# Kernel tuning notes

Measured on AMD Instinct MI355X. Metric: run time of the kernel, lower is better.

The kernel has to match this reference:

```python
import jax, jax.numpy as jnp
import numpy as np

N_NODES = 1048576
N_GRAPHS = 4096
NODES_PER_GRAPH = N_NODES // N_GRAPHS
N_EDGES = 8388608
F_IN = 16
HID = 32


def _glorot(k, shp):
    return jax.random.normal(k, shp, jnp.float32) * np.float32(np.sqrt(2.0 / (shp[-2] + shp[-1])))


def setup_inputs() -> dict:
    key = jax.random.key(0)
    ks = jax.random.split(key, 8)
    d = F_IN + HID  # DCRNN gate convs act on cat([X, H])
    return {
        "x": jax.random.normal(ks[0], (N_NODES, F_IN), jnp.float32),
        "edge_index": jax.random.randint(ks[1], (2, N_EDGES), 0, N_NODES),
        "edge_weight": jax.random.uniform(ks[2], (N_EDGES,), jnp.float32),
        "batch": jnp.repeat(jnp.arange(N_GRAPHS), NODES_PER_GRAPH),
        "W_z": _glorot(ks[3], (2, 1, d, HID)),
        "b_z": jnp.zeros((HID,), jnp.float32),
        "W_r": _glorot(ks[4], (2, 1, d, HID)),
        "b_r": jnp.zeros((HID,), jnp.float32),
        "W_h": _glorot(ks[5], (2, 1, d, HID)),
        "b_h": jnp.zeros((HID,), jnp.float32),
        "W_lin": _glorot(ks[6], (HID, 1)),
        "b_lin": jnp.zeros((1,), jnp.float32),
    }


def _dconv_k1(X, W, b):
    # torch_geometric_temporal DConv with K=1: the diffusion loop never runs,
    # so H = X @ W[0,0] + X @ W[1,0] + b (edge_index/edge_weight unused).
    return X @ (W[0, 0] + W[1, 0]) + b


def reference(x, edge_index, edge_weight, batch, W_z, b_z, W_r, b_r, W_h, b_h, W_lin, b_lin):
    del edge_index, edge_weight  # mathematically unused when K=1
    h0 = jnp.zeros((x.shape[0], HID), x.dtype)  # DCRNN hidden state default
    xh = jnp.concatenate([x, h0], axis=1)
    Z = jax.nn.sigmoid(_dconv_k1(xh, W_z, b_z))
    R = jax.nn.sigmoid(_dconv_k1(xh, W_r, b_r))
    xhr = jnp.concatenate([x, h0 * R], axis=1)
    H_tilde = jnp.tanh(_dconv_k1(xhr, W_h, b_h))
    H = Z * h0 + (1.0 - Z) * H_tilde  # (N, 32)
    h = jax.nn.relu(H)
    h = h @ W_lin + b_lin  # (N, 1)
    # global_mean_pool over per-node graph ids
    sums = jax.ops.segment_sum(h, batch, num_segments=N_GRAPHS)
    cnts = jax.ops.segment_sum(jnp.ones((h.shape[0], 1), h.dtype), batch, num_segments=N_GRAPHS)
    return sums / jnp.maximum(cnts, 1.0)  # (N_GRAPHS, 1)
```

## Files before the change

### kernel.cpp

```cpp
#include <hip/hip_runtime.h>

#define N_NODES   1048576
#define N_GRAPHS  4096
#define NPG       256
#define F_IN      16
#define HID       32

#define WS_FLOATS 1121

__global__ __launch_bounds__(512) void prep_kernel(
    const float* __restrict__ Wz, const float* __restrict__ bz,
    const float* __restrict__ Wh, const float* __restrict__ bh,
    const float* __restrict__ Wlin, const float* __restrict__ blin,
    float* __restrict__ w)
{
    const int t = threadIdx.x;
    if (t < 512) {
        const int c = t >> 4;
        const int r = t & 15;
        const int src = r * HID + c;
        w[t]       = Wz[src] + Wz[1536 + src];
        w[512 + t] = Wh[src] + Wh[1536 + src];
    }
    if (t < HID) {
        w[1024 + t] = bz[t];
        w[1056 + t] = bh[t];
        w[1088 + t] = Wlin[t];
    }
    if (t == 0) w[1120] = blin[0];
}

__device__ __forceinline__ float node_forward(const float xv[F_IN], const float* __restrict__ w)
{
    float acc = 0.0f;
#pragma unroll 4
    for (int c = 0; c < HID; ++c) {
        float az = w[1024 + c];
        float ah = w[1056 + c];
#pragma unroll
        for (int r = 0; r < F_IN; ++r) {
            az = fmaf(xv[r], w[c * 16 + r],        az);
            ah = fmaf(xv[r], w[512 + c * 16 + r],  ah);
        }
        const float z  = 1.0f / (1.0f + __expf(-az));
        const float e  = __expf(2.0f * ah);
        const float th = 1.0f - 2.0f / (e + 1.0f);
        float H = (1.0f - z) * th;
        H = H > 0.0f ? H : 0.0f;
        acc = fmaf(H, w[1088 + c], acc);
    }
    return acc;
}

__device__ __forceinline__ void reduce_and_store(float acc, const float* w, float* out)
{
    const int t = threadIdx.x;
#pragma unroll
    for (int off = 32; off > 0; off >>= 1)
        acc += __shfl_down(acc, off, 64);
    __shared__ float part[4];
    if ((t & 63) == 0) part[t >> 6] = acc;
    __syncthreads();
    if (t == 0) {
        const float s = part[0] + part[1] + part[2] + part[3];
        out[blockIdx.x] = s * (1.0f / (float)NPG) + w[1120];
    }
}

__global__ __launch_bounds__(256) void gcn_main(
    const float* __restrict__ x, const float* __restrict__ w, float* __restrict__ out)
{
    const int node = blockIdx.x * NPG + threadIdx.x;
    const float4* xp = (const float4*)(x + (size_t)node * F_IN);
    const float4 a = xp[0], b = xp[1], c4 = xp[2], d4 = xp[3];
    const float xv[F_IN] = { a.x, a.y, a.z, a.w,  b.x, b.y, b.z, b.w,
                             c4.x, c4.y, c4.z, c4.w,  d4.x, d4.y, d4.z, d4.w };
    const float acc = node_forward(xv, w);
    reduce_and_store(acc, w, out);
}

__global__ __launch_bounds__(256) void gcn_main_lds(
    const float* __restrict__ x,
    const float* __restrict__ Wz, const float* __restrict__ bz,
    const float* __restrict__ Wh, const float* __restrict__ bh,
    const float* __restrict__ Wlin, const float* __restrict__ blin,
    float* __restrict__ out)
{
    __shared__ float w[WS_FLOATS];
    const int t = threadIdx.x;
#pragma unroll
    for (int i = t; i < 512; i += 256) {
        const int c = i >> 4, r = i & 15;
        const int src = r * HID + c;
        w[i]       = Wz[src] + Wz[1536 + src];
        w[512 + i] = Wh[src] + Wh[1536 + src];
    }
    if (t < HID) { w[1024 + t] = bz[t]; w[1056 + t] = bh[t]; w[1088 + t] = Wlin[t]; }
    if (t == 0)  w[1120] = blin[0];
    __syncthreads();

    const int node = blockIdx.x * NPG + t;
    const float4* xp = (const float4*)(x + (size_t)node * F_IN);
    const float4 a = xp[0], b = xp[1], c4 = xp[2], d4 = xp[3];
    const float xv[F_IN] = { a.x, a.y, a.z, a.w,  b.x, b.y, b.z, b.w,
                             c4.x, c4.y, c4.z, c4.w,  d4.x, d4.y, d4.z, d4.w };
    const float acc = node_forward(xv, w);
    reduce_and_store(acc, w, out);
}

extern "C" void kernel_launch(void* const* d_in, const int* in_sizes, int n_in,
                              void* d_out, int out_size, void* d_ws, size_t ws_size,
                              hipStream_t stream)
{
    const float* x    = (const float*)d_in[0];
    const float* Wz   = (const float*)d_in[4];
    const float* bz   = (const float*)d_in[5];
    const float* Wh   = (const float*)d_in[8];
    const float* bh   = (const float*)d_in[9];
    const float* Wlin = (const float*)d_in[10];
    const float* blin = (const float*)d_in[11];
    float* out = (float*)d_out;

    if (ws_size >= WS_FLOATS * sizeof(float)) {
        float* w = (float*)d_ws;
        prep_kernel<<<1, 512, 0, stream>>>(Wz, bz, Wh, bh, Wlin, blin, w);
        gcn_main<<<N_GRAPHS, NPG, 0, stream>>>(x, w, out);
    } else {
        gcn_main_lds<<<N_GRAPHS, NPG, 0, stream>>>(x, Wz, bz, Wh, bh, Wlin, blin, out);
    }
}
```

Baseline: 202.6 us.

## Process four nodes per thread to reuse weight loads across nodes

Each thread now handles four consecutive nodes, loading each weight column once into registers and applying it to all four nodes. This amortises the global/LDS weight reads per FMA and quarters the grid size. Each wavefront now covers exactly one graph, so the shared-memory cross-wave reduction and its barrier go away, and each wave stores its own graph mean. The per-thread x load becomes 16 float4 reads of strided rows, which is less coalesced, and the extra registers may lower occupancy.

```diff
diff --git a/kernel.cpp b/kernel.cpp
--- a/kernel.cpp
+++ b/kernel.cpp
@@ -5,6 +5,7 @@
 #define NPG       256
 #define F_IN      16
 #define HID       32
+#define NODES_PER_THREAD 4
 
 #define WS_FLOATS 1121
 
@@ -15,7 +16,7 @@
     float* __restrict__ w)
 {
     const int t = threadIdx.x;
-    if (t < 512) {
+    {
         const int c = t >> 4;
         const int r = t & 15;
         const int src = r * HID + c;
@@ -30,53 +31,65 @@
     if (t == 0) w[1120] = blin[0];
 }
 
-__device__ __forceinline__ float node_forward(const float xv[F_IN], const float* __restrict__ w)
+__device__ __forceinline__ void gcn_body(
+    const float* __restrict__ x, const float* w, float* __restrict__ out,
+    int block_id, int t)
 {
-    float acc = 0.0f;
-#pragma unroll 4
+    const int base_node = block_id * (NPG * 4) + t * NODES_PER_THREAD;
+    float xv[NODES_PER_THREAD * F_IN];
+    const float4* xp = (const float4*)(x + (size_t)base_node * F_IN);
+#pragma unroll
+    for (int i = 0; i < 16; ++i) {
+        const float4 v = xp[i];
+        xv[i * 4 + 0] = v.x; xv[i * 4 + 1] = v.y;
+        xv[i * 4 + 2] = v.z; xv[i * 4 + 3] = v.w;
+    }
+
+    float acc[NODES_PER_THREAD] = {0.0f, 0.0f, 0.0f, 0.0f};
+
+#pragma unroll 2
     for (int c = 0; c < HID; ++c) {
-        float az = w[1024 + c];
-        float ah = w[1056 + c];
+        float wzc[F_IN], whc[F_IN];
 #pragma unroll
         for (int r = 0; r < F_IN; ++r) {
-            az = fmaf(xv[r], w[c * 16 + r],        az);
-            ah = fmaf(xv[r], w[512 + c * 16 + r],  ah);
+            wzc[r] = w[c * 16 + r];
+            whc[r] = w[512 + c * 16 + r];
         }
-        const float z  = 1.0f / (1.0f + __expf(-az));
-        const float e  = __expf(2.0f * ah);
-        const float th = 1.0f - 2.0f / (e + 1.0f);
-        float H = (1.0f - z) * th;
-        H = H > 0.0f ? H : 0.0f;
-        acc = fmaf(H, w[1088 + c], acc);
+        const float bzc = w[1024 + c];
+        const float bhc = w[1056 + c];
+        const float wlc = w[1088 + c];
+
+#pragma unroll
+        for (int n = 0; n < NODES_PER_THREAD; ++n) {
+            float az = bzc, ah = bhc;
+#pragma unroll
+            for (int r = 0; r < F_IN; ++r) {
+                az = fmaf(xv[n * 16 + r], wzc[r], az);
+                ah = fmaf(xv[n * 16 + r], whc[r], ah);
+            }
+            const float omz = 1.0f / (1.0f + __expf(az));
+            const float eh = __expf(2.0f * ah);
+            const float th = 1.0f - 2.0f / (eh + 1.0f);
+            float H = omz * th;
+            H = H > 0.0f ? H : 0.0f;
+            acc[n] = fmaf(H, wlc, acc[n]);
+        }
     }
-    return acc;
-}
 
-__device__ __forceinline__ void reduce_and_store(float acc, const float* w, float* out)
-{
-    const int t = threadIdx.x;
+    float s = (acc[0] + acc[1]) + (acc[2] + acc[3]);
 #pragma unroll
     for (int off = 32; off > 0; off >>= 1)
-        acc += __shfl_down(acc, off, 64);
-    __shared__ float part[4];
-    if ((t & 63) == 0) part[t >> 6] = acc;
-    __syncthreads();
-    if (t == 0) {
-        const float s = part[0] + part[1] + part[2] + part[3];
-        out[blockIdx.x] = s * (1.0f / (float)NPG) + w[1120];
+        s += __shfl_down(s, off, 64);
+    if ((t & 63) == 0) {
+        const int g = block_id * 4 + (t >> 6);
+        out[g] = s * (1.0f / (float)NPG) + w[1120];
     }
 }
 
 __global__ __launch_bounds__(256) void gcn_main(
     const float* __restrict__ x, const float* __restrict__ w, float* __restrict__ out)
 {
-    const int node = blockIdx.x * NPG + threadIdx.x;
-    const float4* xp = (const float4*)(x + (size_t)node * F_IN);
-    const float4 a = xp[0], b = xp[1], c4 = xp[2], d4 = xp[3];
-    const float xv[F_IN] = { a.x, a.y, a.z, a.w,  b.x, b.y, b.z, b.w,
-                             c4.x, c4.y, c4.z, c4.w,  d4.x, d4.y, d4.z, d4.w };
-    const float acc = node_forward(xv, w);
-    reduce_and_store(acc, w, out);
+    gcn_body(x, w, out, blockIdx.x, threadIdx.x);
 }
 
 __global__ __launch_bounds__(256) void gcn_main_lds(
@@ -98,14 +111,7 @@
     if (t < HID) { w[1024 + t] = bz[t]; w[1056 + t] = bh[t]; w[1088 + t] = Wlin[t]; }
     if (t == 0)  w[1120] = blin[0];
     __syncthreads();
-
-    const int node = blockIdx.x * NPG + t;
-    const float4* xp = (const float4*)(x + (size_t)node * F_IN);
-    const float4 a = xp[0], b = xp[1], c4 = xp[2], d4 = xp[3];
-    const float xv[F_IN] = { a.x, a.y, a.z, a.w,  b.x, b.y, b.z, b.w,
-                             c4.x, c4.y, c4.z, c4.w,  d4.x, d4.y, d4.z, d4.w };
-    const float acc = node_forward(xv, w);
-    reduce_and_store(acc, w, out);
+    gcn_body(x, w, out, blockIdx.x, t);
 }
 
 extern "C" void kernel_launch(void* const* d_in, const int* in_sizes, int n_in,
@@ -121,11 +127,13 @@
     const float* blin = (const float*)d_in[11];
     float* out = (float*)d_out;
 
+    const int n_blocks = N_NODES / (NPG * 4);
+
     if (ws_size >= WS_FLOATS * sizeof(float)) {
         float* w = (float*)d_ws;
         prep_kernel<<<1, 512, 0, stream>>>(Wz, bz, Wh, bh, Wlin, blin, w);
-        gcn_main<<<N_GRAPHS, NPG, 0, stream>>>(x, w, out);
+        gcn_main<<<n_blocks, 256, 0, stream>>>(x, w, out);
     } else {
-        gcn_main_lds<<<N_GRAPHS, NPG, 0, stream>>>(x, Wz, bz, Wh, bh, Wlin, blin, out);
+        gcn_main_lds<<<n_blocks, 256, 0, stream>>>(x, Wz, bz, Wh, bh, Wlin, blin, out);
     }
 }
```

Result: slower. 209.5 us (+3.4%).

## Compute gate projections with fp16 MFMA using split hi/lo inputs

Applied to the files above, without the earlier changes.

Replaces the per-thread scalar FMA loops for the Z and H-tilde projections with MFMA 16x16x32 f16 instructions. Each wave handles 64 nodes over four iterations. The input is split into fp16 high and low parts across the K dimension to keep accuracy close to fp32. Weights are pre-packed into MFMA B fragments and pre-scaled by log2(e), so the gates need only exp2 plus a single reciprocal that fuses sigmoid and tanh. This cuts VALU work, but the fp16 weights add some precision risk and the per-lane x loads are less regular.

```diff
diff --git a/kernel.cpp b/kernel.cpp
--- a/kernel.cpp
+++ b/kernel.cpp
@@ -1,111 +1,157 @@
 #include <hip/hip_runtime.h>
 
-#define N_NODES   1048576
 #define N_GRAPHS  4096
 #define NPG       256
 #define F_IN      16
 #define HID       32
+#define LOG2E     1.4426950408889634f
 
 #define WS_FLOATS 1121
 
-__global__ __launch_bounds__(512) void prep_kernel(
+typedef _Float16 half8   __attribute__((ext_vector_type(8)));
+typedef float    float4v __attribute__((ext_vector_type(4)));
+
+#if __has_builtin(__builtin_amdgcn_exp2f)
+#define EXP2(x) __builtin_amdgcn_exp2f(x)
+#else
+#define EXP2(x) exp2f(x)
+#endif
+
+union FragU { uint4 u; half8 h; };
+
+__device__ __forceinline__ uint4 make_frag(int f, int l,
+    const float* __restrict__ Wz, const float* __restrict__ Wh)
+{
+    const int q = l >> 4, m = l & 15;
+    const int c = (f & 1) * 16 + m;
+    const float s = (f < 2) ? LOG2E : 2.0f * LOG2E;
+    const float* W = (f < 2) ? Wz : Wh;
+    FragU u;
+#pragma unroll
+    for (int j = 0; j < 8; ++j) {
+        const int k = (q & 1) * 8 + j;
+        u.h[j] = (_Float16)((W[k * 32 + c] + W[1536 + k * 32 + c]) * s);
+    }
+    return u.u;
+}
+
+__global__ __launch_bounds__(256) void prep_kernel(
     const float* __restrict__ Wz, const float* __restrict__ bz,
     const float* __restrict__ Wh, const float* __restrict__ bh,
     const float* __restrict__ Wlin, const float* __restrict__ blin,
     float* __restrict__ w)
 {
     const int t = threadIdx.x;
-    if (t < 512) {
-        const int c = t >> 4;
-        const int r = t & 15;
-        const int src = r * HID + c;
-        w[t]       = Wz[src] + Wz[1536 + src];
-        w[512 + t] = Wh[src] + Wh[1536 + src];
-    }
+    ((uint4*)w)[t] = make_frag(t >> 6, t & 63, Wz, Wh);
     if (t < HID) {
-        w[1024 + t] = bz[t];
-        w[1056 + t] = bh[t];
+        w[1024 + t] = bz[t] * LOG2E;
+        w[1056 + t] = bh[t] * (2.0f * LOG2E);
         w[1088 + t] = Wlin[t];
     }
     if (t == 0) w[1120] = blin[0];
 }
 
-__device__ __forceinline__ float node_forward(const float xv[F_IN], const float* __restrict__ w)
+__device__ __forceinline__ float gate_term(float az, float ah, float wl, float osum)
 {
-    float acc = 0.0f;
-#pragma unroll 4
-    for (int c = 0; c < HID; ++c) {
-        float az = w[1024 + c];
-        float ah = w[1056 + c];
-#pragma unroll
-        for (int r = 0; r < F_IN; ++r) {
-            az = fmaf(xv[r], w[c * 16 + r],        az);
-            ah = fmaf(xv[r], w[512 + c * 16 + r],  ah);
-        }
-        const float z  = 1.0f / (1.0f + __expf(-az));
-        const float e  = __expf(2.0f * ah);
-        const float th = 1.0f - 2.0f / (e + 1.0f);
-        float H = (1.0f - z) * th;
-        H = H > 0.0f ? H : 0.0f;
-        acc = fmaf(H, w[1088 + c], acc);
-    }
-    return acc;
+    const float e1 = EXP2(az);
+    const float e2 = EXP2(fminf(ah, 126.0f));
+    const float r  = __builtin_amdgcn_rcpf((1.0f + e1) * (e2 + 1.0f));
+    float v = (e2 - 1.0f) * r;
+    v = v > 0.0f ? v : 0.0f;
+    return fmaf(v, wl, osum);
 }
 
-__device__ __forceinline__ void reduce_and_store(float acc, const float* w, float* out)
+__device__ __forceinline__ void gcn_body(const float* __restrict__ x,
+                                         const float* __restrict__ w,
+                                         float* __restrict__ out, int g, int t)
 {
-    const int t = threadIdx.x;
+    const int lane = t & 63, wv = t >> 6;
+    const int q = lane >> 4, m = lane & 15;
+
+    const uint4* bq = (const uint4*)w;
+    FragU u0, u1, u2, u3;
+    u0.u = bq[lane];       u1.u = bq[64 + lane];
+    u2.u = bq[128 + lane]; u3.u = bq[192 + lane];
+    const half8 Bz0 = u0.h, Bz1 = u1.h, Bh0 = u2.h, Bh1 = u3.h;
+
+    const float bz0 = w[1024 + m], bz1 = w[1040 + m];
+    const float bh0 = w[1056 + m], bh1 = w[1072 + m];
+    const float wl0 = w[1088 + m], wl1 = w[1104 + m];
+
+    const float* xw = x + ((size_t)g * NPG + wv * 64 + m) * F_IN + (q & 1) * 8;
+    float4 c0 = *(const float4*)(xw);
+    float4 c1 = *(const float4*)(xw + 4);
+    const bool lo_lane = (q >= 2);
+    float osum = 0.0f;
+
+#pragma unroll
+    for (int it = 0; it < 4; ++it) {
+        float4 n0 = c0, n1 = c1;
+        if (it < 3) {
+            n0 = *(const float4*)(xw + (it + 1) * 256);
+            n1 = *(const float4*)(xw + (it + 1) * 256 + 4);
+        }
+        const float xf[8] = { c0.x, c0.y, c0.z, c0.w, c1.x, c1.y, c1.z, c1.w };
+        half8 A;
+#pragma unroll
+        for (int j = 0; j < 8; ++j) {
+            _Float16 h = (_Float16)xf[j];
+            if (lo_lane) h = (_Float16)(xf[j] - (float)h);
+            A[j] = h;
+        }
+
+        float4v az0 = { bz0, bz0, bz0, bz0 };
+        float4v az1 = { bz1, bz1, bz1, bz1 };
+        float4v ah0 = { bh0, bh0, bh0, bh0 };
+        float4v ah1 = { bh1, bh1, bh1, bh1 };
+        az0 = __builtin_amdgcn_mfma_f32_16x16x32_f16(A, Bz0, az0, 0, 0, 0);
+        ah0 = __builtin_amdgcn_mfma_f32_16x16x32_f16(A, Bh0, ah0, 0, 0, 0);
+        az1 = __builtin_amdgcn_mfma_f32_16x16x32_f16(A, Bz1, az1, 0, 0, 0);
+        ah1 = __builtin_amdgcn_mfma_f32_16x16x32_f16(A, Bh1, ah1, 0, 0, 0);
+
+#pragma unroll
+        for (int i = 0; i < 4; ++i) {
+            osum = gate_term(az0[i], ah0[i], wl0, osum);
+            osum = gate_term(az1[i], ah1[i], wl1, osum);
+        }
+        c0 = n0; c1 = n1;
+    }
+
 #pragma unroll
     for (int off = 32; off > 0; off >>= 1)
-        acc += __shfl_down(acc, off, 64);
+        osum += __shfl_down(osum, off, 64);
     __shared__ float part[4];
-    if ((t & 63) == 0) part[t >> 6] = acc;
+    if (lane == 0) part[wv] = osum;
     __syncthreads();
-    if (t == 0) {
-        const float s = part[0] + part[1] + part[2] + part[3];
-        out[blockIdx.x] = s * (1.0f / (float)NPG) + w[1120];
-    }
+    if (t == 0)
+        out[g] = (part[0] + part[1] + part[2] + part[3]) * (1.0f / (float)NPG)
+               + w[1120];
 }
 
-__global__ __launch_bounds__(256) void gcn_main(
+__global__ __launch_bounds__(256, 6) void gcn_main(
     const float* __restrict__ x, const float* __restrict__ w, float* __restrict__ out)
 {
-    const int node = blockIdx.x * NPG + threadIdx.x;
-    const float4* xp = (const float4*)(x + (size_t)node * F_IN);
-    const float4 a = xp[0], b = xp[1], c4 = xp[2], d4 = xp[3];
-    const float xv[F_IN] = { a.x, a.y, a.z, a.w,  b.x, b.y, b.z, b.w,
-                             c4.x, c4.y, c4.z, c4.w,  d4.x, d4.y, d4.z, d4.w };
-    const float acc = node_forward(xv, w);
-    reduce_and_store(acc, w, out);
+    gcn_body(x, w, out, blockIdx.x, threadIdx.x);
 }
 
-__global__ __launch_bounds__(256) void gcn_main_lds(
+__global__ __launch_bounds__(256, 6) void gcn_main_lds(
     const float* __restrict__ x,
     const float* __restrict__ Wz, const float* __restrict__ bz,
     const float* __restrict__ Wh, const float* __restrict__ bh,
     const float* __restrict__ Wlin, const float* __restrict__ blin,
     float* __restrict__ out)
 {
-    __shared__ float w[WS_FLOATS];
+    __shared__ __attribute__((aligned(16))) float w[WS_FLOATS];
     const int t = threadIdx.x;
-#pragma unroll
-    for (int i = t; i < 512; i += 256) {
-        const int c = i >> 4, r = i & 15;
-        const int src = r * HID + c;
-        w[i]       = Wz[src] + Wz[1536 + src];
-        w[512 + i] = Wh[src] + Wh[1536 + src];
+    ((uint4*)w)[t] = make_frag(t >> 6, t & 63, Wz, Wh);
+    if (t < HID) {
+        w[1024 + t] = bz[t] * LOG2E;
+        w[1056 + t] = bh[t] * (2.0f * LOG2E);
+        w[1088 + t] = Wlin[t];
     }
-    if (t < HID) { w[1024 + t] = bz[t]; w[1056 + t] = bh[t]; w[1088 + t] = Wlin[t]; }
-    if (t == 0)  w[1120] = blin[0];
+    if (t == 0) w[1120] = blin[0];
     __syncthreads();
-
-    const int node = blockIdx.x * NPG + t;
-    const float4* xp = (const float4*)(x + (size_t)node * F_IN);
-    const float4 a = xp[0], b = xp[1], c4 = xp[2], d4 = xp[3];
-    const float xv[F_IN] = { a.x, a.y, a.z, a.w,  b.x, b.y, b.z, b.w,
-                             c4.x, c4.y, c4.z, c4.w,  d4.x, d4.y, d4.z, d4.w };
-    const float acc = node_forward(xv, w);
-    reduce_and_store(acc, w, out);
+    gcn_body(x, w, out, blockIdx.x, t);
 }
 
 extern "C" void kernel_launch(void* const* d_in, const int* in_sizes, int n_in,
@@ -123,7 +169,7 @@
 
     if (ws_size >= WS_FLOATS * sizeof(float)) {
         float* w = (float*)d_ws;
-        prep_kernel<<<1, 512, 0, stream>>>(Wz, bz, Wh, bh, Wlin, blin, w);
+        prep_kernel<<<1, 256, 0, stream>>>(Wz, bz, Wh, bh, Wlin, blin, w);
         gcn_main<<<N_GRAPHS, NPG, 0, stream>>>(x, w, out);
     } else {
         gcn_main_lds<<<N_GRAPHS, NPG, 0, stream>>>(x, Wz, bz, Wh, bh, Wlin, blin, out);
```

Result: faster. 166.1 us (-18.0%).
